# Kernel optimization log

Hardware: AMD Instinct MI355X
Metric: run time of the kernel (lower is better)

The kernel has to match this reference:

```python
import jax, jax.numpy as jnp
import numpy as np

N_HEADS = 16
NEG_INF = -1e9


def setup_inputs() -> dict:
    key = jax.random.key(0)
    k1, k2, k3 = jax.random.split(key, 3)
    B, S, D = 4, 4096, 1024
    x = jax.random.normal(k1, (B, S, D), dtype=jnp.float32)
    # GPT-2-style init scale
    w_qkv = jax.random.normal(k2, (D, 3 * D), dtype=jnp.float32) * 0.02
    b_qkv = jnp.zeros((3 * D,), dtype=jnp.float32)
    w_o = jax.random.normal(k3, (D, D), dtype=jnp.float32) * 0.02
    b_o = jnp.zeros((D,), dtype=jnp.float32)
    return {"x": x, "w_qkv": w_qkv, "b_qkv": b_qkv, "w_o": w_o, "b_o": b_o,
            "window_size": 512}


def reference(x, w_qkv, b_qkv, w_o, b_o, window_size):
    B, S, D = x.shape
    W = window_size
    n_win = S // W  # loop `for i in range(0, S, W)` with S % W == 0
    H = N_HEADS
    dh = D // H

    # All windows are independent -> fold them into the batch dim instead of a
    # Python loop (same math as looping + concat along seq dim).
    xw = x.reshape(B * n_win, W, D)

    qkv = xw @ w_qkv + b_qkv                      # [BN, W, 3D]
    q, k, v = jnp.split(qkv, 3, axis=-1)
    # [BN, H, W, dh]
    q = q.reshape(-1, W, H, dh).transpose(0, 2, 1, 3)
    k = k.reshape(-1, W, H, dh).transpose(0, 2, 1, 3)
    v = v.reshape(-1, W, H, dh).transpose(0, 2, 1, 3)

    scale = 1.0 / jnp.sqrt(jnp.asarray(dh, dtype=x.dtype))
    scores = jnp.einsum('bhqd,bhkd->bhqk', q, k) * scale  # [BN, H, W, W]
    causal = jnp.tril(jnp.ones((W, W), dtype=bool))       # GPT-2 causal mask (per window)
    scores = jnp.where(causal, scores, NEG_INF)
    attn = jax.nn.softmax(scores, axis=-1)

    out = jnp.einsum('bhqk,bhkd->bhqd', attn, v)          # [BN, H, W, dh]
    out = out.transpose(0, 2, 1, 3).reshape(-1, W, D)     # [BN, W, D]
    out = out @ w_o + b_o
    return out.reshape(B, S, D)
```

## Files before the change

### kernel.cpp

```cpp
#include <hip/hip_runtime.h>


typedef unsigned short u16;
typedef unsigned int u32;
typedef __attribute__((ext_vector_type(8))) short bf16x8;
typedef __attribute__((ext_vector_type(4))) float f32x4;

__device__ __forceinline__ float bf2f(u16 v) {
  union { u32 u; float f; } t; t.u = ((u32)v) << 16; return t.f;
}
__device__ __forceinline__ u16 f2bf(float f) {
  union { float f; u32 u; } t; t.f = f;
  u32 u = t.u + 0x7fffu + ((t.u >> 16) & 1u);
  return (u16)(u >> 16);
}
__device__ __forceinline__ void g2lds16(const void* g, void* l) {
  __builtin_amdgcn_global_load_lds((const __attribute__((address_space(1))) void*)g,
                                   (__attribute__((address_space(3))) void*)l,
                                   16, 0, 0);
}

__global__ __launch_bounds__(256) void canon_x(
    const float* __restrict__ xf, u16* __restrict__ xb) {
  size_t i = ((size_t)blockIdx.x * 256 + threadIdx.x) * 8;
  float4 a = *(const float4*)(xf + i);
  float4 b = *(const float4*)(xf + i + 4);
  u16 o[8] = { f2bf(a.x), f2bf(a.y), f2bf(a.z), f2bf(a.w),
               f2bf(b.x), f2bf(b.y), f2bf(b.z), f2bf(b.w) };
  *(bf16x8*)(xb + i) = *(bf16x8*)o;
}

__global__ __launch_bounds__(256) void transpose_w(
    const float* __restrict__ in, u16* __restrict__ out, int R, int C) {
  __shared__ u16 tile[32][33];
  int c0 = blockIdx.x * 32, r0 = blockIdx.y * 32;
  int tx = threadIdx.x & 31, ty = threadIdx.x >> 5;
#pragma unroll
  for (int i = 0; i < 32; i += 8)
    tile[ty + i][tx] = f2bf(in[(size_t)(r0 + ty + i) * C + c0 + tx]);
  __syncthreads();
#pragma unroll
  for (int i = 0; i < 32; i += 8)
    out[(size_t)(c0 + ty + i) * R + r0 + tx] = tile[tx][ty + i];
}

__global__ __launch_bounds__(256) void transpose_v(
    const u16* __restrict__ qkv, u16* __restrict__ vt) {
  __shared__ u16 tile[32][33];
  int bh = blockIdx.z, bn = bh >> 4, h = bh & 15;
  int t0 = blockIdx.x * 32, d0 = blockIdx.y * 32;
  int tx = threadIdx.x & 31, ty = threadIdx.x >> 5;
  const u16* src = qkv + (size_t)(bn * 512) * 3072 + 2048 + h * 64;
#pragma unroll
  for (int i = 0; i < 32; i += 8)
    tile[ty + i][tx] = src[(size_t)(t0 + ty + i) * 3072 + d0 + tx];
  __syncthreads();
  u16* dst = vt + ((size_t)bh * 64 + d0) * 512 + t0;
#pragma unroll
  for (int i = 0; i < 32; i += 8)
    dst[(size_t)(ty + i) * 512 + tx] = tile[tx][ty + i];
}

template <typename OutT>
__global__ __launch_bounds__(512, 2) void gemm_bt_bias(
    const u16* __restrict__ A, const u16* __restrict__ Bt,
    const float* __restrict__ bias, OutT* __restrict__ C,
    int M, int N, int K) {
  __shared__ __align__(16) u16 As[2][256 * 64];
  __shared__ __align__(16) u16 Bs[2][256 * 64];
  const int tid = threadIdx.x;
  const int wave = tid >> 6, lane = tid & 63;
  const int quad = lane >> 4, l16 = lane & 15;
  const int wr = wave >> 2, wc = wave & 3;

  const int nbx = gridDim.x;
  const int ntot = nbx * gridDim.y;
  const int flat = blockIdx.y * nbx + blockIdx.x;
  const int swz = (flat & 7) * (ntot >> 3) + (flat >> 3);
  const int m0 = (swz / nbx) * 256, n0 = (swz % nbx) * 256;

  const int rS = tid >> 3, cS = tid & 7;

#define STAGE(KT, BUF)                                                        \
  {                                                                           \
    const int k0_ = (KT) * 64;                                                \
    _Pragma("unroll")                                                         \
    for (int it = 0; it < 4; ++it) {                                          \
      const int row = it * 64 + rS;                                           \
      const int sg = (cS ^ (row & 7)) * 8;                                    \
      g2lds16(A + (size_t)(m0 + row) * K + k0_ + sg,                          \
              &As[BUF][(size_t)(it * 512 + tid) * 8]);                        \
      g2lds16(Bt + (size_t)(n0 + row) * K + k0_ + sg,                         \
              &Bs[BUF][(size_t)(it * 512 + tid) * 8]);                        \
    }                                                                         \
  }

  f32x4 acc[8][4] = {};

  const int NT = K >> 6;
  STAGE(0, 0);
  if (NT > 1) STAGE(1, 1);

  for (int t = 0; t < NT; ++t) {
    if (t + 1 < NT) { asm volatile("s_waitcnt vmcnt(8)" ::: "memory"); }
    else            { asm volatile("s_waitcnt vmcnt(0)" ::: "memory"); }
    __builtin_amdgcn_s_barrier();
    __builtin_amdgcn_sched_barrier(0);

    const u16* Ab = &As[t & 1][0];
    const u16* Bb = &Bs[t & 1][0];

    bf16x8 bfr[2][4];
#pragma unroll
    for (int ks = 0; ks < 2; ++ks)
#pragma unroll
      for (int ni = 0; ni < 4; ++ni) {
        int row = wc * 64 + ni * 16 + l16;
        bfr[ks][ni] = *(const bf16x8*)(Bb + row * 64 + (((ks * 4 + quad) ^ (row & 7)) * 8));
      }

#pragma unroll
    for (int p = 0; p < 4; ++p) {
      bf16x8 afr[2][2];
#pragma unroll
      for (int mm = 0; mm < 2; ++mm)
#pragma unroll
        for (int ks = 0; ks < 2; ++ks) {
          int row = wr * 128 + (p * 2 + mm) * 16 + l16;
          afr[mm][ks] = *(const bf16x8*)(Ab + row * 64 + (((ks * 4 + quad) ^ (row & 7)) * 8));
        }
      __builtin_amdgcn_s_setprio(1);
#pragma unroll
      for (int mm = 0; mm < 2; ++mm)
#pragma unroll
        for (int ni = 0; ni < 4; ++ni)
#pragma unroll
          for (int ks = 0; ks < 2; ++ks)
            acc[p * 2 + mm][ni] = __builtin_amdgcn_mfma_f32_16x16x32_bf16(
                afr[mm][ks], bfr[ks][ni], acc[p * 2 + mm][ni], 0, 0, 0);
      __builtin_amdgcn_s_setprio(0);
      __builtin_amdgcn_s_barrier();
    }
    __builtin_amdgcn_sched_barrier(0);
    if (t + 2 < NT) STAGE(t + 2, t & 1);
  }
#undef STAGE

#pragma unroll
  for (int ni = 0; ni < 4; ++ni) {
    int col = n0 + wc * 64 + ni * 16 + l16;
    float bv = bias[col];
#pragma unroll
    for (int mi = 0; mi < 8; ++mi) {
      int row0 = m0 + wr * 128 + mi * 16 + quad * 4;
#pragma unroll
      for (int r = 0; r < 4; ++r) {
        float v = acc[mi][ni][r] + bv;
        if constexpr (sizeof(OutT) == 2)
          C[(size_t)(row0 + r) * N + col] = f2bf(v);
        else
          C[(size_t)(row0 + r) * N + col] = v;
      }
    }
  }
}

__global__ __launch_bounds__(256, 2) void attn_win(
    const u16* __restrict__ qkv, const u16* __restrict__ vt,
    u16* __restrict__ attn) {
  __shared__ __align__(16) u16 Ks[128 * 64];
  __shared__ __align__(16) u16 Vs[64 * 128];
  __shared__ __align__(16) u16 Ps[4][16 * 128];

  const int qt = blockIdx.x, h = blockIdx.y, bn = blockIdx.z;
  const int bh = bn * 16 + h;
  const int tid = threadIdx.x;
  const int wave = tid >> 6, lane = tid & 63;
  const int quad = lane >> 4, l16 = lane & 15;
  const int t0 = bn * 512 + qt * 128;

  bf16x8 aq[2][2];
#pragma unroll
  for (int mi = 0; mi < 2; ++mi)
#pragma unroll
    for (int ks = 0; ks < 2; ++ks)
      aq[mi][ks] = *(const bf16x8*)(
          qkv + (size_t)(t0 + wave * 32 + mi * 16 + l16) * 3072 + h * 64 + ks * 32 + quad * 8);

  const int rk0 = tid >> 3, ck0 = tid & 7;
  const int rv0 = tid >> 4, cv0 = tid & 15;

#define STAGE_K(JT)                                                           \
  {                                                                           \
    const int tk_ = bn * 512 + (JT) * 128;                                    \
    _Pragma("unroll")                                                         \
    for (int it = 0; it < 4; ++it) {                                          \
      int rk = it * 32 + rk0;                                                 \
      const u16* gk = qkv + (size_t)(tk_ + rk) * 3072 + 1024 + h * 64 +       \
                      ((ck0 ^ (rk & 7)) * 8);                                 \
      g2lds16(gk, Ks + (size_t)(it * 256 + wave * 64) * 8);                   \
    }                                                                         \
  }
#define STAGE_V(JT)                                                           \
  {                                                                           \
    _Pragma("unroll")                                                         \
    for (int it = 0; it < 4; ++it) {                                          \
      int rv = it * 16 + rv0;                                                 \
      const u16* gv = vt + ((size_t)bh * 64 + rv) * 512 + (JT) * 128 +        \
                      ((cv0 ^ (rv & 15)) * 8);                                \
      g2lds16(gv, Vs + (size_t)(it * 256 + wave * 64) * 8);                   \
    }                                                                         \
  }

  STAGE_K(0);
  STAGE_V(0);
  asm volatile("s_waitcnt vmcnt(4)" ::: "memory");
  __builtin_amdgcn_s_barrier();
  __builtin_amdgcn_sched_barrier(0);

  float mrun[2][4], lrun[2][4];
  f32x4 o[2][4] = {};
#pragma unroll
  for (int mi = 0; mi < 2; ++mi)
#pragma unroll
    for (int r = 0; r < 4; ++r) { mrun[mi][r] = -1e30f; lrun[mi][r] = 0.f; }

  const float cexp = 0.18033688011112042f;

  u16* pw = &Ps[wave][0];

  for (int j = 0; j <= qt; ++j) {
    f32x4 s[2][8] = {};
    __builtin_amdgcn_s_setprio(1);
#pragma unroll
    for (int ks = 0; ks < 2; ++ks) {
#pragma unroll
      for (int ni = 0; ni < 8; ++ni) {
        int n = ni * 16 + l16;
        bf16x8 bk = *(const bf16x8*)(Ks + n * 64 + (((ks * 4 + quad) ^ (n & 7)) * 8));
        s[0][ni] = __builtin_amdgcn_mfma_f32_16x16x32_bf16(aq[0][ks], bk, s[0][ni], 0, 0, 0);
        s[1][ni] = __builtin_amdgcn_mfma_f32_16x16x32_bf16(aq[1][ks], bk, s[1][ni], 0, 0, 0);
      }
    }
    __builtin_amdgcn_s_setprio(0);

    __builtin_amdgcn_s_barrier();
    __builtin_amdgcn_sched_barrier(0);
    if (j < qt) STAGE_K(j + 1);

    const bool diag = (j == qt);
#pragma unroll
    for (int mi = 0; mi < 2; ++mi) {
#pragma unroll
      for (int r = 0; r < 4; ++r) {
        int m = wave * 32 + mi * 16 + quad * 4 + r;
        float rmax = -1e30f;
#pragma unroll
        for (int ni = 0; ni < 8; ++ni) {
          float v = s[mi][ni][r] * cexp;
          if (diag && (ni * 16 + l16 > m)) v = -1e30f;
          s[mi][ni][r] = v;
          rmax = fmaxf(rmax, v);
        }
        rmax = fmaxf(rmax, __shfl_xor(rmax, 1));
        rmax = fmaxf(rmax, __shfl_xor(rmax, 2));
        rmax = fmaxf(rmax, __shfl_xor(rmax, 4));
        rmax = fmaxf(rmax, __shfl_xor(rmax, 8));
        float mnew = fmaxf(mrun[mi][r], rmax);
        float alpha = exp2f(mrun[mi][r] - mnew);
        mrun[mi][r] = mnew;
        float rsum = 0.f;
#pragma unroll
        for (int ni = 0; ni < 8; ++ni) {
          float pv = exp2f(s[mi][ni][r] - mnew);
          s[mi][ni][r] = pv;
          rsum += pv;
        }
        rsum += __shfl_xor(rsum, 1);
        rsum += __shfl_xor(rsum, 2);
        rsum += __shfl_xor(rsum, 4);
        rsum += __shfl_xor(rsum, 8);
        lrun[mi][r] = lrun[mi][r] * alpha + rsum;
#pragma unroll
        for (int di = 0; di < 4; ++di) o[mi][di][r] *= alpha;
      }
    }

    if (j < qt) { asm volatile("s_waitcnt vmcnt(4)" ::: "memory"); }
    else        { asm volatile("s_waitcnt vmcnt(0)" ::: "memory"); }
    __builtin_amdgcn_s_barrier();
    __builtin_amdgcn_sched_barrier(0);

#pragma unroll
    for (int mi = 0; mi < 2; ++mi) {
#pragma unroll
      for (int ni = 0; ni < 8; ++ni)
#pragma unroll
        for (int r = 0; r < 4; ++r) {
          int row = quad * 4 + r;
          int col = ni * 16 + l16;
          int phys = (col >> 3) ^ row;
          pw[row * 128 + phys * 8 + (col & 7)] = f2bf(s[mi][ni][r]);
        }

      __builtin_amdgcn_s_setprio(1);
#pragma unroll
      for (int ksv = 0; ksv < 4; ++ksv) {
        bf16x8 ap = *(const bf16x8*)(pw + l16 * 128 + (((ksv * 4 + quad) ^ l16) * 8));
#pragma unroll
        for (int di = 0; di < 4; ++di) {
          int n = di * 16 + l16;
          bf16x8 bv = *(const bf16x8*)(Vs + n * 128 + (((ksv * 4 + quad) ^ (n & 15)) * 8));
          o[mi][di] = __builtin_amdgcn_mfma_f32_16x16x32_bf16(ap, bv, o[mi][di], 0, 0, 0);
        }
      }
      __builtin_amdgcn_s_setprio(0);
    }

    asm volatile("s_waitcnt vmcnt(0)" ::: "memory");
    __builtin_amdgcn_s_barrier();
    __builtin_amdgcn_sched_barrier(0);
    if (j < qt) STAGE_V(j + 1);
  }
#undef STAGE_K
#undef STAGE_V

#pragma unroll
  for (int mi = 0; mi < 2; ++mi)
#pragma unroll
    for (int r = 0; r < 4; ++r) {
      float inv = 1.0f / lrun[mi][r];
      int trow = t0 + wave * 32 + mi * 16 + quad * 4 + r;
#pragma unroll
      for (int di = 0; di < 4; ++di)
        attn[(size_t)trow * 1024 + h * 64 + di * 16 + l16] = f2bf(o[mi][di][r] * inv);
    }
}

extern "C" void kernel_launch(void* const* d_in, const int* in_sizes, int n_in,
                              void* d_out, int out_size, void* d_ws, size_t ws_size,
                              hipStream_t stream) {
  (void)in_sizes; (void)n_in; (void)out_size; (void)ws_size;
  const float* x     = (const float*)d_in[0];
  const float* w_qkv = (const float*)d_in[1];
  const float* b_qkv = (const float*)d_in[2];
  const float* w_o   = (const float*)d_in[3];
  const float* b_o   = (const float*)d_in[4];
  float* out = (float*)d_out;

  char* ws = (char*)d_ws;
  u16* qkv   = (u16*)(ws + 0);
  u16* vtb   = (u16*)(ws + 100663296);
  u16* attnb = (u16*)(ws + 134217728);
  u16* xb    = (u16*)(ws + 167772160);
  u16* wqkvT = (u16*)(ws + 201326592);
  u16* woT   = (u16*)(ws + 207618048);

  canon_x<<<8192, 256, 0, stream>>>(x, xb);
  transpose_w<<<dim3(96, 32), 256, 0, stream>>>(w_qkv, wqkvT, 1024, 3072);
  transpose_w<<<dim3(32, 32), 256, 0, stream>>>(w_o, woT, 1024, 1024);

  gemm_bt_bias<u16><<<dim3(12, 64), 512, 0, stream>>>(
      xb, wqkvT, b_qkv, qkv, 16384, 3072, 1024);
  transpose_v<<<dim3(16, 2, 512), 256, 0, stream>>>(qkv, vtb);
  attn_win<<<dim3(4, 16, 32), 256, 0, stream>>>(qkv, vtb, attnb);
  gemm_bt_bias<float><<<dim3(4, 64), 512, 0, stream>>>(
      attnb, woT, b_o, out, 16384, 1024, 1024);
}
```

Before: 452.3 us.

## Interleave A-tile prefetch per phase in GEMM and relax occupancy hint

```diff
diff --git a/kernel.cpp b/kernel.cpp
--- a/kernel.cpp
+++ b/kernel.cpp
@@ -62,7 +62,7 @@
 }
 
 template <typename OutT>
-__global__ __launch_bounds__(512, 2) void gemm_bt_bias(
+__global__ __launch_bounds__(512, 1) void gemm_bt_bias(
     const u16* __restrict__ A, const u16* __restrict__ Bt,
     const float* __restrict__ bias, OutT* __restrict__ C,
     int M, int N, int K) {
@@ -79,27 +79,33 @@
   const int swz = (flat & 7) * (ntot >> 3) + (flat >> 3);
   const int m0 = (swz / nbx) * 256, n0 = (swz % nbx) * 256;
 
-  const int rS = tid >> 3, cS = tid & 7;
-
-#define STAGE(KT, BUF)                                                        \
-  {                                                                           \
-    const int k0_ = (KT) * 64;                                                \
-    _Pragma("unroll")                                                         \
-    for (int it = 0; it < 4; ++it) {                                          \
-      const int row = it * 64 + rS;                                           \
-      const int sg = (cS ^ (row & 7)) * 8;                                    \
-      g2lds16(A + (size_t)(m0 + row) * K + k0_ + sg,                          \
-              &As[BUF][(size_t)(it * 512 + tid) * 8]);                        \
-      g2lds16(Bt + (size_t)(n0 + row) * K + k0_ + sg,                         \
-              &Bs[BUF][(size_t)(it * 512 + tid) * 8]);                        \
-    }                                                                         \
-  }
+  const int r8 = tid >> 3;
+  const int sgm = ((tid & 7) ^ (r8 & 7)) * 8;
+  const u16* gA = A + (size_t)(m0 + r8) * K + sgm;
+  const u16* gB = Bt + (size_t)(n0 + r8) * K + sgm;
+  const int rl = r8 & 31;
+  const int halfsel = tid >> 8;
+  const u16* gAp = A + (size_t)(m0 + halfsel * 128 + rl) * K + sgm;
+  const int ldsAp = halfsel * 8192 + (wave & 3) * 512 + lane * 8;
+
+#define STAGE_FULL(KT, BUF)                                                   \
+  { _Pragma("unroll") for (int l = 0; l < 4; ++l) {                           \
+      g2lds16(gA + (size_t)l * 64 * K + (KT),                                 \
+              &As[BUF][((size_t)l * 512 + tid) * 8]);                         \
+      g2lds16(gB + (size_t)l * 64 * K + (KT),                                 \
+              &Bs[BUF][((size_t)l * 512 + tid) * 8]); } }
+#define STAGE_A_PHASE(P, KT, BUF)                                             \
+  g2lds16(gAp + (size_t)(P) * 32 * K + (KT), &As[BUF][ldsAp + (P) * 2048]);
+#define STAGE_B_FULL(KT, BUF)                                                 \
+  { _Pragma("unroll") for (int l = 0; l < 4; ++l)                             \
+      g2lds16(gB + (size_t)l * 64 * K + (KT),                                 \
+              &Bs[BUF][((size_t)l * 512 + tid) * 8]); }
 
   f32x4 acc[8][4] = {};
-
   const int NT = K >> 6;
-  STAGE(0, 0);
-  if (NT > 1) STAGE(1, 1);
+
+  STAGE_FULL(0, 0);
+  STAGE_FULL(64, 1);
 
   for (int t = 0; t < NT; ++t) {
     if (t + 1 < NT) { asm volatile("s_waitcnt vmcnt(8)" ::: "memory"); }
@@ -109,6 +115,9 @@
 
     const u16* Ab = &As[t & 1][0];
     const u16* Bb = &Bs[t & 1][0];
+    const int kt2 = (t + 2) * 64;
+    const int buf = t & 1;
+    const bool st = (t + 2 < NT);
 
     bf16x8 bfr[2][4];
 #pragma unroll
@@ -140,11 +149,14 @@
                 afr[mm][ks], bfr[ks][ni], acc[p * 2 + mm][ni], 0, 0, 0);
       __builtin_amdgcn_s_setprio(0);
       __builtin_amdgcn_s_barrier();
-    }
-    __builtin_amdgcn_sched_barrier(0);
-    if (t + 2 < NT) STAGE(t + 2, t & 1);
-  }
-#undef STAGE
+      __builtin_amdgcn_sched_barrier(0);
+      if (st) { STAGE_A_PHASE(p, kt2, buf); }
+    }
+    if (st) { STAGE_B_FULL(kt2, buf); }
+  }
+#undef STAGE_FULL
+#undef STAGE_A_PHASE
+#undef STAGE_B_FULL
 
 #pragma unroll
   for (int ni = 0; ni < 4; ++ni) {
```

Result: slower. 468.0 us (+3.5%).

## Interleave half-tile global-to-LDS loads with MFMA phases in GEMM

Applied to the files above, without the earlier changes.

```diff
diff --git a/kernel.cpp b/kernel.cpp
--- a/kernel.cpp
+++ b/kernel.cpp
@@ -62,12 +62,12 @@
 }
 
 template <typename OutT>
-__global__ __launch_bounds__(512, 2) void gemm_bt_bias(
+__global__ __launch_bounds__(512) void gemm_bt_bias(
     const u16* __restrict__ A, const u16* __restrict__ Bt,
     const float* __restrict__ bias, OutT* __restrict__ C,
     int M, int N, int K) {
-  __shared__ __align__(16) u16 As[2][256 * 64];
-  __shared__ __align__(16) u16 Bs[2][256 * 64];
+  __shared__ __align__(16) u16 As[2][2][128 * 64];
+  __shared__ __align__(16) u16 Bs[2][2][128 * 64];
   const int tid = threadIdx.x;
   const int wave = tid >> 6, lane = tid & 63;
   const int quad = lane >> 4, l16 = lane & 15;
@@ -79,72 +79,96 @@
   const int swz = (flat & 7) * (ntot >> 3) + (flat >> 3);
   const int m0 = (swz / nbx) * 256, n0 = (swz % nbx) * 256;
 
-  const int rS = tid >> 3, cS = tid & 7;
-
-#define STAGE(KT, BUF)                                                        \
+  const int rr = tid >> 3;
+  const int sc0 = ((tid & 7) ^ (rr & 7)) * 8;
+
+#define STAGE_HALF(SRC, DST, ROWBASE, KT)                                     \
   {                                                                           \
-    const int k0_ = (KT) * 64;                                                \
-    _Pragma("unroll")                                                         \
-    for (int it = 0; it < 4; ++it) {                                          \
-      const int row = it * 64 + rS;                                           \
-      const int sg = (cS ^ (row & 7)) * 8;                                    \
-      g2lds16(A + (size_t)(m0 + row) * K + k0_ + sg,                          \
-              &As[BUF][(size_t)(it * 512 + tid) * 8]);                        \
-      g2lds16(Bt + (size_t)(n0 + row) * K + k0_ + sg,                         \
-              &Bs[BUF][(size_t)(it * 512 + tid) * 8]);                        \
-    }                                                                         \
-  }
+    g2lds16((SRC) + (size_t)((ROWBASE) + rr) * K + (KT) * 64 + sc0,           \
+            (DST) + (size_t)tid * 8);                                         \
+    g2lds16((SRC) + (size_t)((ROWBASE) + rr + 64) * K + (KT) * 64 + sc0,      \
+            (DST) + (size_t)(tid + 512) * 8);                                 \
+  }
+
+  const int NT = K >> 6;
+  const int NI = NT >> 1;
+
+  STAGE_HALF(A,  &As[0][0][0], m0,       0);
+  STAGE_HALF(A,  &As[0][1][0], m0 + 128, 0);
+  STAGE_HALF(Bt, &Bs[0][0][0], n0,       0);
+  STAGE_HALF(Bt, &Bs[0][1][0], n0 + 128, 0);
+  STAGE_HALF(Bt, &Bs[1][0][0], n0,       1);
+  STAGE_HALF(Bt, &Bs[1][1][0], n0 + 128, 1);
+  asm volatile("s_waitcnt vmcnt(4)" ::: "memory");
+  __builtin_amdgcn_s_barrier();
+  __builtin_amdgcn_sched_barrier(0);
 
   f32x4 acc[8][4] = {};
-
-  const int NT = K >> 6;
-  STAGE(0, 0);
-  if (NT > 1) STAGE(1, 1);
-
-  for (int t = 0; t < NT; ++t) {
-    if (t + 1 < NT) { asm volatile("s_waitcnt vmcnt(8)" ::: "memory"); }
-    else            { asm volatile("s_waitcnt vmcnt(0)" ::: "memory"); }
-    __builtin_amdgcn_s_barrier();
-    __builtin_amdgcn_sched_barrier(0);
-
-    const u16* Ab = &As[t & 1][0];
-    const u16* Bb = &Bs[t & 1][0];
-
-    bf16x8 bfr[2][4];
-#pragma unroll
-    for (int ks = 0; ks < 2; ++ks)
-#pragma unroll
-      for (int ni = 0; ni < 4; ++ni) {
-        int row = wc * 64 + ni * 16 + l16;
-        bfr[ks][ni] = *(const bf16x8*)(Bb + row * 64 + (((ks * 4 + quad) ^ (row & 7)) * 8));
-      }
-
-#pragma unroll
-    for (int p = 0; p < 4; ++p) {
+  bf16x8 bfr[2][4];
+
+  for (int i = 0; i < NI; ++i) {
+#pragma unroll
+    for (int p = 0; p < 8; ++p) {
+      const int tt = 2 * i + (p >> 2);
+      const int bb = tt & 1;
+      const int q = p & 3;
+
+      if (q == 0) {
+        const u16* Bb = &Bs[bb][wc >> 1][0];
+        const int rbase = (wc & 1) * 64;
+#pragma unroll
+        for (int ks = 0; ks < 2; ++ks)
+#pragma unroll
+          for (int ni = 0; ni < 4; ++ni) {
+            int row = rbase + ni * 16 + l16;
+            bfr[ks][ni] = *(const bf16x8*)(Bb + row * 64 + (((ks * 4 + quad) ^ (row & 7)) * 8));
+          }
+      }
       bf16x8 afr[2][2];
+      {
+        const u16* Ab = &As[bb][wr][0];
+#pragma unroll
+        for (int mm = 0; mm < 2; ++mm)
+#pragma unroll
+          for (int ks = 0; ks < 2; ++ks) {
+            int row = q * 32 + mm * 16 + l16;
+            afr[mm][ks] = *(const bf16x8*)(Ab + row * 64 + (((ks * 4 + quad) ^ (row & 7)) * 8));
+          }
+      }
+
+      switch (p) {
+        case 0: if (2*i+1 < NT) STAGE_HALF(A,  &As[1][0][0], m0,       2*i+1); break;
+        case 1: if (2*i+1 < NT) STAGE_HALF(A,  &As[1][1][0], m0 + 128, 2*i+1); break;
+        case 2: if (2*i+2 < NT) STAGE_HALF(Bt, &Bs[0][0][0], n0,       2*i+2); break;
+        case 3: if (2*i+2 < NT) STAGE_HALF(Bt, &Bs[0][1][0], n0 + 128, 2*i+2); break;
+        case 4: if (2*i+2 < NT) STAGE_HALF(A,  &As[0][0][0], m0,       2*i+2); break;
+        case 5: if (2*i+2 < NT) STAGE_HALF(A,  &As[0][1][0], m0 + 128, 2*i+2); break;
+        case 6: if (2*i+3 < NT) STAGE_HALF(Bt, &Bs[1][0][0], n0,       2*i+3); break;
+        case 7: if (2*i+3 < NT) STAGE_HALF(Bt, &Bs[1][1][0], n0 + 128, 2*i+3); break;
+      }
+
+      __builtin_amdgcn_s_barrier();
+      asm volatile("s_waitcnt lgkmcnt(0)" ::: "memory");
+      __builtin_amdgcn_sched_barrier(0);
+      __builtin_amdgcn_s_setprio(1);
 #pragma unroll
       for (int mm = 0; mm < 2; ++mm)
 #pragma unroll
-        for (int ks = 0; ks < 2; ++ks) {
-          int row = wr * 128 + (p * 2 + mm) * 16 + l16;
-          afr[mm][ks] = *(const bf16x8*)(Ab + row * 64 + (((ks * 4 + quad) ^ (row & 7)) * 8));
-        }
-      __builtin_amdgcn_s_setprio(1);
-#pragma unroll
-      for (int mm = 0; mm < 2; ++mm)
-#pragma unroll
         for (int ni = 0; ni < 4; ++ni)
 #pragma unroll
           for (int ks = 0; ks < 2; ++ks)
-            acc[p * 2 + mm][ni] = __builtin_amdgcn_mfma_f32_16x16x32_bf16(
-                afr[mm][ks], bfr[ks][ni], acc[p * 2 + mm][ni], 0, 0, 0);
+            acc[q * 2 + mm][ni] = __builtin_amdgcn_mfma_f32_16x16x32_bf16(
+                afr[mm][ks], bfr[ks][ni], acc[q * 2 + mm][ni], 0, 0, 0);
       __builtin_amdgcn_s_setprio(0);
+      if (p == 3 || p == 7) {
+        if (i + 1 < NI) { asm volatile("s_waitcnt vmcnt(4)" ::: "memory"); }
+        else            { asm volatile("s_waitcnt vmcnt(0)" ::: "memory"); }
+      }
       __builtin_amdgcn_s_barrier();
-    }
-    __builtin_amdgcn_sched_barrier(0);
-    if (t + 2 < NT) STAGE(t + 2, t & 1);
-  }
-#undef STAGE
+      __builtin_amdgcn_sched_barrier(0);
+    }
+  }
+#undef STAGE_HALF
 
 #pragma unroll
   for (int ni = 0; ni < 4; ++ni) {
```

After: 434.3 us. 4.0% less time.
